# Kernel tuning notes

Hardware: AMD Instinct MI355X
Metric: run time of the kernel (lower is better)

Reference implementation:

```python
import jax, jax.numpy as jnp
import numpy as np

N_HEAD = 16
HEAD_SIZE = 64

def setup_inputs() -> dict:
    key = jax.random.key(0)
    ks = jax.random.split(key, 5)
    B, T, C = 2, 2048, 1024
    s = 0.02
    return {
        "x": jax.random.normal(ks[0], (B, T, C), dtype=jnp.float32),
        "We": jax.random.normal(ks[1], (3 * C, C), dtype=jnp.float32) * s,
        "be": jax.random.normal(ks[2], (3 * C,), dtype=jnp.float32) * s,
        "Wp": jax.random.normal(ks[3], (C, C), dtype=jnp.float32) * s,
        "bp": jax.random.normal(ks[4], (C,), dtype=jnp.float32) * s,
    }

def reference(x, We, be, Wp, bp):
    B, T, C = x.shape
    H, D = N_HEAD, HEAD_SIZE
    qkv = x @ We.T + be                      # [B,T,3C]
    q, k, v = jnp.split(qkv, 3, axis=-1)
    # [B,H,T,D]
    q = q.reshape(B, T, H, D).transpose(0, 2, 1, 3)
    k = k.reshape(B, T, H, D).transpose(0, 2, 1, 3)
    v = v.reshape(B, T, H, D).transpose(0, 2, 1, 3)
    scale = 1.0 / jnp.sqrt(jnp.asarray(D, dtype=x.dtype))
    att = jnp.einsum('bhqd,bhkd->bhqk', q, k) * scale
    causal = jnp.tril(jnp.ones((T, T), dtype=bool))
    att = jnp.where(causal, att, -jnp.inf)
    att = jax.nn.softmax(att, axis=-1)
    y = jnp.einsum('bhqk,bhkd->bhqd', att, v)   # [B,H,T,D]
    y = y.transpose(0, 2, 1, 3).reshape(B, T, C)
    return y @ Wp.T + bp
```

## Files before the change

### kernel.cpp

```cpp
#include <hip/hip_runtime.h>
#include <hip/hip_bf16.h>
#include <stdint.h>
#include <stddef.h>

typedef short s8v __attribute__((ext_vector_type(8)));
typedef float f4v __attribute__((ext_vector_type(4)));

__device__ inline float b2f(short s) {
    union { unsigned u; float f; } x;
    x.u = ((unsigned)(unsigned short)s) << 16;
    return x.f;
}
__device__ inline short f2b(float f) {
    union { float f; unsigned u; } x;
    x.f = f;
    unsigned r = x.u + 0x7FFF + ((x.u >> 16) & 1);
    return (short)(r >> 16);
}

__device__ __forceinline__ void gl16(const short* g, short* l) {
    __builtin_amdgcn_global_load_lds(
        (const __attribute__((address_space(1))) void*)g,
        (__attribute__((address_space(3))) void*)l,
        16, 0, 0);
}

__global__ __launch_bounds__(256) void convert_bf16(
    const void* s0, short* d0, size_t c0,
    const void* s1, short* d1, size_t c1,
    const void* s2, short* d2, size_t c2,
    const void* s3, short* d3, size_t c3,
    const void* s4, short* d4, size_t c4,
    int* __restrict__ flagout)
{
    int hit = 0;
    const unsigned* xw = (const unsigned*)s0;
    for (int i = threadIdx.x & 63; i < 1024; i += 64) {
        unsigned e = ((xw[i] & 0xFFFFu) >> 7) & 0xFFu;
        if (e >= 0x8Au) hit = 1;
    }
    const bool f32 = (__ballot(hit != 0) != 0ull);
    if (blockIdx.x == 0 && threadIdx.x == 0) *flagout = f32 ? 1 : 0;

    const void* srcs[5] = {s0, s1, s2, s3, s4};
    short* dsts[5] = {d0, d1, d2, d3, d4};
    size_t cnts[5] = {c0, c1, c2, c3, c4};
    size_t total = c0 + c1 + c2 + c3 + c4;
    size_t stride = (size_t)gridDim.x * blockDim.x;
    for (size_t c = (size_t)blockIdx.x * blockDim.x + threadIdx.x; c < total; c += stride) {
        size_t r = c; int s = 0;
        while (r >= cnts[s]) { r -= cnts[s]; s++; }
        short* d = dsts[s] + r * 8;
        if (f32) {
            const float* p = (const float*)srcs[s] + r * 8;
            f4v a = *(const f4v*)p;
            f4v b = *(const f4v*)(p + 4);
            s8v v;
            v[0] = f2b(a[0]); v[1] = f2b(a[1]); v[2] = f2b(a[2]); v[3] = f2b(a[3]);
            v[4] = f2b(b[0]); v[5] = f2b(b[1]); v[6] = f2b(b[2]); v[7] = f2b(b[3]);
            *(s8v*)d = v;
        } else {
            *(s8v*)d = *(const s8v*)((const short*)srcs[s] + r * 8);
        }
    }
}

#define BKK 64

template<int QKV, int TBM, int TBN, int MINW>
__global__ __launch_bounds__(256, MINW) void gemm_bt_bias(
    const short* __restrict__ A,
    const short* __restrict__ B,
    const short* __restrict__ bias,
    void* __restrict__ C,
    short* __restrict__ vT,
    int M, int N, int K, int ldc,
    const int* __restrict__ flagp, int oDyn)
{
    const bool of32 = oDyn && (*flagp != 0);
    const int MT = TBM / 32, NT = TBN / 32;

    __shared__ __align__(16) short smem[(TBM + TBN) * BKK];
    short* sA = smem;
    short* sB = smem + TBM * BKK;

    const int tid  = threadIdx.x;
    const int lane = tid & 63;
    const int w    = tid >> 6;
    const int wm   = (w >> 1) * (TBM / 2);
    const int wn   = (w & 1) * (TBN / 2);
    const int quad = lane >> 4;
    const int l16  = lane & 15;

    const int m0 = blockIdx.y * TBM;
    const int n0 = blockIdx.x * TBN;

    f4v acc[MT][NT];
    const f4v vzero = {0.0f, 0.0f, 0.0f, 0.0f};
#pragma unroll
    for (int i = 0; i < MT; i++)
#pragma unroll
        for (int j = 0; j < NT; j++) acc[i][j] = vzero;

    const int ACH = TBM * 8;
    for (int k0 = 0; k0 < K; k0 += BKK) {
        __syncthreads();
#pragma unroll
        for (int i = 0; i < (TBM + TBN) / 32; i++) {
            int c  = i * 256 + tid;
            int cb = i * 256 + (tid & 192);
            if (c < ACH) {
                int r = c >> 3, kk = (c & 7) * 8;
                gl16(A + (size_t)(m0 + r) * K + k0 + kk, sA + cb * 8);
            } else {
                int c2 = c - ACH, cb2 = cb - ACH;
                int r = c2 >> 3, kk = (c2 & 7) * 8;
                gl16(B + (size_t)(n0 + r) * K + k0 + kk, sB + cb2 * 8);
            }
        }
        __syncthreads();
#pragma unroll
        for (int s = 0; s < 2; s++) {
            s8v af[MT], bf[NT];
#pragma unroll
            for (int t = 0; t < MT; t++)
                af[t] = *(const s8v*)(sA + (wm + t * 16 + l16) * BKK + s * 32 + quad * 8);
#pragma unroll
            for (int t = 0; t < NT; t++)
                bf[t] = *(const s8v*)(sB + (wn + t * 16 + l16) * BKK + s * 32 + quad * 8);
#pragma unroll
            for (int mt = 0; mt < MT; mt++)
#pragma unroll
                for (int nt = 0; nt < NT; nt++)
                    acc[mt][nt] = __builtin_amdgcn_mfma_f32_16x16x32_bf16(
                        af[mt], bf[nt], acc[mt][nt], 0, 0, 0);
        }
    }

    if (QKV && n0 >= 2048) {
        static_assert(!QKV || TBM == 64, "V transpose assumes TBM==64");
        __syncthreads();
#pragma unroll
        for (int nt = 0; nt < NT; nt++) {
            int nl = wn + nt * 16 + l16;
            float bv = b2f(bias[n0 + nl]);
#pragma unroll
            for (int mt = 0; mt < MT; mt++)
#pragma unroll
                for (int r = 0; r < 4; r++) {
                    int ml = wm + mt * 16 + quad * 4 + r;
                    smem[nl * 72 + ml] = f2b(acc[mt][nt][r] + bv);
                }
        }
        __syncthreads();
        int nl = tid >> 1, half = tid & 1;
        int n = n0 + nl;
        int h = (n - 2048) >> 6, d = n & 63;
        int bq = m0 >> 11;
        short* dst = vT + (((size_t)(bq * 16 + h)) * 64 + d) * 2048 + (m0 & 2047) + half * 32;
        const short* src = smem + nl * 72 + half * 32;
#pragma unroll
        for (int j = 0; j < 4; j++)
            *(s8v*)(dst + j * 8) = *(const s8v*)(src + j * 8);
    } else if (QKV) {
        const float osc = (n0 < 1024) ? 0.125f : 1.0f;
        __syncthreads();
#pragma unroll
        for (int nt = 0; nt < NT; nt++) {
            int nl = wn + nt * 16 + l16;
            float bv = b2f(bias[n0 + nl]);
#pragma unroll
            for (int mt = 0; mt < MT; mt++)
#pragma unroll
                for (int r = 0; r < 4; r++) {
                    int ml = wm + mt * 16 + quad * 4 + r;
                    smem[ml * 144 + nl] = f2b((acc[mt][nt][r] + bv) * osc);
                }
        }
        __syncthreads();
#pragma unroll
        for (int i = 0; i < 4; i++) {
            int c = i * 256 + tid;
            int m = c >> 4, ncol = (c & 15) * 8;
            *(s8v*)((short*)C + (size_t)(m0 + m) * ldc + n0 + ncol) =
                *(const s8v*)(smem + m * 144 + ncol);
        }
    } else {
#pragma unroll
        for (int nt = 0; nt < NT; nt++) {
            int n = n0 + wn + nt * 16 + l16;
            float bv = b2f(bias[n]);
#pragma unroll
            for (int mt = 0; mt < MT; mt++) {
#pragma unroll
                for (int r = 0; r < 4; r++) {
                    int m = m0 + wm + mt * 16 + quad * 4 + r;
                    float v = acc[mt][nt][r] + bv;
                    if (of32) ((float*)C)[(size_t)m * ldc + n] = v;
                    else      ((short*)C)[(size_t)m * ldc + n] = f2b(v);
                }
            }
        }
    }
}

#define LP 72

template<int PARTS>
__global__ __launch_bounds__(256) void attn_flash(
    const short* __restrict__ qk,
    const short* __restrict__ vt,
    short* __restrict__ y,
    short* __restrict__ Opart,
    float* __restrict__ Lpart)
{
    const int T = 2048, LDQ = 2048;
    __shared__ __align__(16) short sK[64 * LP];
    __shared__ __align__(16) short sVT[64 * LP];
    __shared__ __align__(16) short sP[4][16 * LP];

    const int tid  = threadIdx.x;
    const int lane = tid & 63;
    const int w    = tid >> 6;
    const int quad = lane >> 4;
    const int l16  = lane & 15;

    int part, qt, bh, u;
    if (PARTS == 2) {
        part = blockIdx.x & 1;
        int rest = blockIdx.x >> 1;
        qt = 31 - (rest >> 5);
        bh = rest & 31;
        u  = bh * 32 + qt;
    } else {
        part = 0;
        qt = 31 - (blockIdx.x >> 5);
        bh = blockIdx.x & 31;
        u  = 0;
    }
    const int b = bh >> 4;
    const int h = bh & 15;

    const int n    = qt + 1;
    const int half = (n + 1) >> 1;
    const int klo  = (PARTS == 2 && part) ? half : 0;
    const int khi  = (PARTS == 2 && !part) ? half : n;

    if (PARTS == 2 && klo >= khi) {
        s8v z;
#pragma unroll
        for (int j = 0; j < 8; j++) z[j] = 0;
        s8v* ob = (s8v*)(Opart + ((size_t)(part * 1024 + u)) * 4096);
        for (int i = tid; i < 512; i += 256) ob[i] = z;
        if (tid < 64) Lpart[(size_t)(part * 1024 + u) * 64 + tid] = 0.0f;
        return;
    }

    const size_t qkbase = (size_t)b * T * LDQ;
    const short* Kbase  = qk + qkbase + 1024 + h * 64;
    const short* Vbase  = vt + (size_t)bh * 64 * 2048;

    s8v qf[2];
    {
        int qrow = qt * 64 + w * 16 + l16;
        const short* qp = qk + qkbase + (size_t)qrow * LDQ + h * 64 + quad * 8;
        qf[0] = *(const s8v*)(qp);
        qf[1] = *(const s8v*)(qp + 32);
    }

    const f4v vzero = {0.0f, 0.0f, 0.0f, 0.0f};
    f4v o[4];
#pragma unroll
    for (int i = 0; i < 4; i++) o[i] = vzero;
    float lsum[4] = {0.0f, 0.0f, 0.0f, 0.0f};

    for (int kt = klo; kt < khi; kt++) {
        __syncthreads();
#pragma unroll
        for (int i = 0; i < 2; i++) {
            int c = i * 256 + tid;
            int r = c >> 3, dd = (c & 7) * 8;
            s8v kv = *(const s8v*)(Kbase + (size_t)(kt * 64 + r) * LDQ + dd);
            s8v vv = *(const s8v*)(Vbase + (size_t)r * 2048 + kt * 64 + dd);
            *(s8v*)(sK  + r * LP + dd) = kv;
            *(s8v*)(sVT + r * LP + dd) = vv;
        }
        __syncthreads();

        f4v sacc[4];
#pragma unroll
        for (int nt = 0; nt < 4; nt++) {
            sacc[nt] = vzero;
            s8v kf0 = *(const s8v*)(sK + (nt * 16 + l16) * LP + quad * 8);
            s8v kf1 = *(const s8v*)(sK + (nt * 16 + l16) * LP + 32 + quad * 8);
            sacc[nt] = __builtin_amdgcn_mfma_f32_16x16x32_bf16(qf[0], kf0, sacc[nt], 0, 0, 0);
            sacc[nt] = __builtin_amdgcn_mfma_f32_16x16x32_bf16(qf[1], kf1, sacc[nt], 0, 0, 0);
        }

        short* pp = sP[w];
        const bool diag = (kt == qt);
#pragma unroll
        for (int nt = 0; nt < 4; nt++) {
#pragma unroll
            for (int r = 0; r < 4; r++) {
                float p = __expf(sacc[nt][r]);
                if (diag) {
                    int q = w * 16 + quad * 4 + r;
                    int k = nt * 16 + l16;
                    if (k > q) p = 0.0f;
                }
                union { float f; unsigned u; } c; c.f = p;
                short p16 = (short)(c.u >> 16);
                c.u &= 0xFFFF0000u;
                lsum[r] += c.f;
                pp[(quad * 4 + r) * LP + nt * 16 + l16] = p16;
            }
        }
        __syncthreads();

        s8v pf0 = *(const s8v*)(pp + l16 * LP + quad * 8);
        s8v pf1 = *(const s8v*)(pp + l16 * LP + 32 + quad * 8);
#pragma unroll
        for (int dt = 0; dt < 4; dt++) {
            s8v vf0 = *(const s8v*)(sVT + (dt * 16 + l16) * LP + quad * 8);
            s8v vf1 = *(const s8v*)(sVT + (dt * 16 + l16) * LP + 32 + quad * 8);
            o[dt] = __builtin_amdgcn_mfma_f32_16x16x32_bf16(pf0, vf0, o[dt], 0, 0, 0);
            o[dt] = __builtin_amdgcn_mfma_f32_16x16x32_bf16(pf1, vf1, o[dt], 0, 0, 0);
        }
    }

#pragma unroll
    for (int r = 0; r < 4; r++) {
        float s = lsum[r];
        s += __shfl_xor(s, 1, 64);
        s += __shfl_xor(s, 2, 64);
        s += __shfl_xor(s, 4, 64);
        s += __shfl_xor(s, 8, 64);
        lsum[r] = s;
    }

    if (PARTS == 2) {
        short* ob = Opart + ((size_t)(part * 1024 + u)) * 4096;
#pragma unroll
        for (int dt = 0; dt < 4; dt++)
#pragma unroll
            for (int r = 0; r < 4; r++)
                ob[(w * 16 + quad * 4 + r) * 64 + dt * 16 + l16] = f2b(o[dt][r]);
        if (l16 == 0) {
#pragma unroll
            for (int r = 0; r < 4; r++)
                Lpart[(size_t)(part * 1024 + u) * 64 + w * 16 + quad * 4 + r] = lsum[r];
        }
    } else {
#pragma unroll
        for (int r = 0; r < 4; r++) lsum[r] = 1.0f / lsum[r];
#pragma unroll
        for (int dt = 0; dt < 4; dt++)
#pragma unroll
            for (int r = 0; r < 4; r++) {
                int qrow = qt * 64 + w * 16 + quad * 4 + r;
                int d = dt * 16 + l16;
                y[((size_t)b * T + qrow) * 1024 + h * 64 + d] = f2b(o[dt][r] * lsum[r]);
            }
    }
}

__global__ __launch_bounds__(256) void attn_combine(
    const short* __restrict__ Opart,
    const float* __restrict__ Lpart,
    short* __restrict__ y)
{
    const int u  = blockIdx.x;
    const int bh = u >> 5, qt = u & 31;
    const int b = bh >> 4, h = bh & 15;
    const int t = threadIdx.x;
    const int q = t >> 2, dg = (t & 3) * 16;

    float l = Lpart[(size_t)u * 64 + q] + Lpart[(size_t)(1024 + u) * 64 + q];
    float rl = 1.0f / l;
    const short* p0 = Opart + (size_t)u * 4096 + q * 64 + dg;
    const short* p1 = Opart + (size_t)(1024 + u) * 4096 + q * 64 + dg;
    short* yo = y + ((size_t)b * 2048 + qt * 64 + q) * 1024 + h * 64 + dg;
#pragma unroll
    for (int hv = 0; hv < 2; hv++) {
        s8v a = *(const s8v*)(p0 + hv * 8);
        s8v c = *(const s8v*)(p1 + hv * 8);
        s8v r;
#pragma unroll
        for (int j = 0; j < 8; j++) r[j] = f2b((b2f(a[j]) + b2f(c[j])) * rl);
        *(s8v*)(yo + hv * 8) = r;
    }
}

extern "C" void kernel_launch(void* const* d_in, const int* in_sizes, int n_in,
                              void* d_out, int out_size, void* d_ws, size_t ws_size,
                              hipStream_t stream)
{
    char* p = (char*)d_ws;
    int*   flag = (int*)p;                 p += 16;
    short* qk   = (short*)p;               p += (size_t)4096 * 2048 * 2;
    short* vT   = (short*)p;               p += (size_t)32 * 64 * 2048 * 2;
    short* xb   = (short*)p;               p += (size_t)4096 * 1024 * 2;
    short* Web  = (short*)p;               p += (size_t)3072 * 1024 * 2;
    short* Wpb  = (short*)p;               p += (size_t)1024 * 1024 * 2;
    short* beb  = (short*)p;               p += 3072 * 2;
    short* bpb  = (short*)p;               p += 1024 * 2;
    short* Opart = (short*)p;              p += (size_t)2 * 1024 * 4096 * 2;
    float* Lpart = (float*)p;              p += (size_t)2 * 1024 * 64 * 4;
    short* y = xb;
    const size_t need = (size_t)(p - (char*)d_ws);
    const bool split = (ws_size >= need);

    convert_bf16<<<dim3(4098), 256, 0, stream>>>(
        d_in[0], xb,  (size_t)4096 * 1024 / 8,
        d_in[1], Web, (size_t)3072 * 1024 / 8,
        d_in[2], beb, (size_t)3072 / 8,
        d_in[3], Wpb, (size_t)1024 * 1024 / 8,
        d_in[4], bpb, (size_t)1024 / 8,
        flag);

    gemm_bt_bias<1, 64, 128, 6><<<dim3(3072 / 128, 4096 / 64), 256, 0, stream>>>(
        xb, Web, beb, qk, vT, 4096, 3072, 1024, 2048, flag, 0);

    if (split) {
        attn_flash<2><<<dim3(2048), 256, 0, stream>>>(qk, vT, nullptr, Opart, Lpart);
        attn_combine<<<dim3(1024), 256, 0, stream>>>(Opart, Lpart, y);
    } else {
        attn_flash<1><<<dim3(1024), 256, 0, stream>>>(qk, vT, y, nullptr, nullptr);
    }

    gemm_bt_bias<0, 128, 64, 2><<<dim3(1024 / 64, 4096 / 128), 256, 0, stream>>>(
        y, Wpb, bpb, d_out, nullptr, 4096, 1024, 1024, 1024, flag, 1);
}
```

Baseline: 203.7 us.

## Split-K the output projection with a bf16 partial-sum combine kernel

Replaces the 128x64 output-projection GEMM with a 64x64-tile, split-K=2 GEMM that writes bf16 partial sums into the reused qk buffer, then adds a proj_combine kernel that sums the partials, adds the bias and writes fp32 or bf16 output. The aim is more blocks and higher occupancy for the small N=1024 projection. The cost is an extra launch, extra global traffic and rounding of the partials to bf16. It also removes a __syncthreads between writing P to LDS and reading it in the attention kernel, which relies on each wave only reading its own P slice.

```diff
diff --git a/kernel.cpp b/kernel.cpp
--- a/kernel.cpp
+++ b/kernel.cpp
@@ -67,7 +67,7 @@
 
 #define BKK 64
 
-template<int QKV, int TBM, int TBN, int MINW>
+template<int MODE, int TBM, int TBN, int SPLITK, int MINW>
 __global__ __launch_bounds__(256, MINW) void gemm_bt_bias(
     const short* __restrict__ A,
     const short* __restrict__ B,
@@ -79,6 +79,7 @@
 {
     const bool of32 = oDyn && (*flagp != 0);
     const int MT = TBM / 32, NT = TBN / 32;
+    const int RST = TBN + (TBN == 128 ? 16 : 8);
 
     __shared__ __align__(16) short smem[(TBM + TBN) * BKK];
     short* sA = smem;
@@ -94,6 +95,8 @@
 
     const int m0 = blockIdx.y * TBM;
     const int n0 = blockIdx.x * TBN;
+    const int kz = blockIdx.z;
+    const int KS = K / SPLITK;
 
     f4v acc[MT][NT];
     const f4v vzero = {0.0f, 0.0f, 0.0f, 0.0f};
@@ -103,7 +106,7 @@
         for (int j = 0; j < NT; j++) acc[i][j] = vzero;
 
     const int ACH = TBM * 8;
-    for (int k0 = 0; k0 < K; k0 += BKK) {
+    for (int k0 = kz * KS; k0 < (kz + 1) * KS; k0 += BKK) {
         __syncthreads();
 #pragma unroll
         for (int i = 0; i < (TBM + TBN) / 32; i++) {
@@ -137,8 +140,7 @@
         }
     }
 
-    if (QKV && n0 >= 2048) {
-        static_assert(!QKV || TBM == 64, "V transpose assumes TBM==64");
+    if (MODE == 1 && n0 >= 2048) {
         __syncthreads();
 #pragma unroll
         for (int nt = 0; nt < NT; nt++) {
@@ -162,28 +164,30 @@
 #pragma unroll
         for (int j = 0; j < 4; j++)
             *(s8v*)(dst + j * 8) = *(const s8v*)(src + j * 8);
-    } else if (QKV) {
-        const float osc = (n0 < 1024) ? 0.125f : 1.0f;
+    } else if (MODE == 1 || MODE == 2) {
+        const float osc = (MODE == 1 && n0 < 1024) ? 0.125f : 1.0f;
+        short* Cp = (short*)C + (MODE == 2 ? (size_t)kz * M * ldc : 0);
         __syncthreads();
 #pragma unroll
         for (int nt = 0; nt < NT; nt++) {
             int nl = wn + nt * 16 + l16;
-            float bv = b2f(bias[n0 + nl]);
+            float bv = (MODE == 1) ? b2f(bias[n0 + nl]) : 0.0f;
 #pragma unroll
             for (int mt = 0; mt < MT; mt++)
 #pragma unroll
                 for (int r = 0; r < 4; r++) {
                     int ml = wm + mt * 16 + quad * 4 + r;
-                    smem[ml * 144 + nl] = f2b((acc[mt][nt][r] + bv) * osc);
+                    smem[ml * RST + nl] = f2b((acc[mt][nt][r] + bv) * osc);
                 }
         }
         __syncthreads();
-#pragma unroll
-        for (int i = 0; i < 4; i++) {
+        const int CPR = TBN / 8;
+#pragma unroll
+        for (int i = 0; i < TBM * CPR / 256; i++) {
             int c = i * 256 + tid;
-            int m = c >> 4, ncol = (c & 15) * 8;
-            *(s8v*)((short*)C + (size_t)(m0 + m) * ldc + n0 + ncol) =
-                *(const s8v*)(smem + m * 144 + ncol);
+            int m = c / CPR, ncol = (c % CPR) * 8;
+            *(s8v*)(Cp + (size_t)(m0 + m) * ldc + n0 + ncol) =
+                *(const s8v*)(smem + m * RST + ncol);
         }
     } else {
 #pragma unroll
@@ -201,6 +205,34 @@
                 }
             }
         }
+    }
+}
+
+__global__ __launch_bounds__(256) void proj_combine(
+    const short* __restrict__ P,
+    const short* __restrict__ bias,
+    void* __restrict__ out,
+    const int* __restrict__ flagp)
+{
+    const bool of32 = (*flagp != 0);
+    size_t idx = ((size_t)blockIdx.x * 256 + threadIdx.x) * 8;
+    int n = (int)(idx & 1023);
+    s8v a = *(const s8v*)(P + idx);
+    s8v c = *(const s8v*)(P + (size_t)4096 * 1024 + idx);
+    s8v bb = *(const s8v*)(bias + n);
+    float v[8];
+#pragma unroll
+    for (int j = 0; j < 8; j++) v[j] = b2f(a[j]) + b2f(c[j]) + b2f(bb[j]);
+    if (of32) {
+        f4v r0 = {v[0], v[1], v[2], v[3]};
+        f4v r1 = {v[4], v[5], v[6], v[7]};
+        *(f4v*)((float*)out + idx) = r0;
+        *(f4v*)((float*)out + idx + 4) = r1;
+    } else {
+        s8v r;
+#pragma unroll
+        for (int j = 0; j < 8; j++) r[j] = f2b(v[j]);
+        *(s8v*)((short*)out + idx) = r;
     }
 }
 
@@ -316,7 +348,6 @@
                 pp[(quad * 4 + r) * LP + nt * 16 + l16] = p16;
             }
         }
-        __syncthreads();
 
         s8v pf0 = *(const s8v*)(pp + l16 * LP + quad * 8);
         s8v pf1 = *(const s8v*)(pp + l16 * LP + 32 + quad * 8);
@@ -408,6 +439,7 @@
     short* Opart = (short*)p;              p += (size_t)2 * 1024 * 4096 * 2;
     float* Lpart = (float*)p;              p += (size_t)2 * 1024 * 64 * 4;
     short* y = xb;
+    short* Ppart = qk;
     const size_t need = (size_t)(p - (char*)d_ws);
     const bool split = (ws_size >= need);
 
@@ -419,16 +451,18 @@
         d_in[4], bpb, (size_t)1024 / 8,
         flag);
 
-    gemm_bt_bias<1, 64, 128, 6><<<dim3(3072 / 128, 4096 / 64), 256, 0, stream>>>(
+    gemm_bt_bias<1, 64, 128, 1, 6><<<dim3(24, 64), 256, 0, stream>>>(
         xb, Web, beb, qk, vT, 4096, 3072, 1024, 2048, flag, 0);
 
     if (split) {
         attn_flash<2><<<dim3(2048), 256, 0, stream>>>(qk, vT, nullptr, Opart, Lpart);
         attn_combine<<<dim3(1024), 256, 0, stream>>>(Opart, Lpart, y);
+        gemm_bt_bias<2, 64, 64, 2, 8><<<dim3(16, 64, 2), 256, 0, stream>>>(
+            y, Wpb, bpb, Ppart, nullptr, 4096, 1024, 1024, 1024, flag, 1);
+        proj_combine<<<dim3(2048), 256, 0, stream>>>(Ppart, bpb, d_out, flag);
     } else {
         attn_flash<1><<<dim3(1024), 256, 0, stream>>>(qk, vT, y, nullptr, nullptr);
-    }
-
-    gemm_bt_bias<0, 128, 64, 2><<<dim3(1024 / 64, 4096 / 128), 256, 0, stream>>>(
-        y, Wpb, bpb, d_out, nullptr, 4096, 1024, 1024, 1024, flag, 1);
-}
+        gemm_bt_bias<0, 128, 64, 1, 2><<<dim3(16, 32), 256, 0, stream>>>(
+            y, Wpb, bpb, d_out, nullptr, 4096, 1024, 1024, 1024, flag, 1);
+    }
+}
```

Result: slower. 212.3 us (+4.2%).
